# Kernel optimization log

Hardware: AMD Instinct MI355X
Metric: run time of the kernel (lower is better)

Reference implementation:

```python
import jax, jax.numpy as jnp
import numpy as np
from jax import lax

NEG = -1e30  # log-space 'zero' that stays finite for stable grads


def _logadd3(a, b, c):
    m = jnp.maximum(jnp.maximum(a, b), c)
    return m + jnp.log(jnp.exp(a - m) + jnp.exp(b - m) + jnp.exp(c - m))


def _logadd2(a, b):
    m = jnp.maximum(a, b)
    return m + jnp.log(jnp.exp(a - m) + jnp.exp(b - m))


def setup_inputs() -> dict:
    key = jax.random.key(0)
    k1, k2, k3 = jax.random.split(key, 3)
    B, T, V, L = 64, 2000, 512, 200
    logits = jax.random.normal(k1, (B, T, V), dtype=jnp.float32)
    # keep input lengths well above 2*L+1 so all paths are feasible
    input_lengths = (T - jax.random.randint(k2, (B,), 0, 256)).astype(jnp.int32)
    targets = jax.random.randint(k3, (B, L), 0, V, dtype=jnp.int32)  # 0 == pad == blank
    return {"logits": logits, "input_lengths": input_lengths, "targets": targets}


def ctc_loss_sum(logits, input_lengths, targets):
    B, T, V = logits.shape
    L = targets.shape[1]
    S = 2 * L + 1

    lp = jax.nn.log_softmax(logits, axis=-1)  # [B,T,V]

    # compact nonzero targets per row (masked_select equivalent, fixed shape)
    mask = targets != 0
    tlen = mask.sum(-1)  # [B] target_lengths
    pos = jnp.where(mask, jnp.cumsum(mask, axis=1) - 1, L)
    compact = jnp.zeros_like(targets).at[jnp.arange(B)[:, None], pos].set(targets, mode="drop")

    # extended label sequence: blank, y1, blank, y2, ..., blank  -> [B,S]
    s_idx = jnp.arange(S)
    lab_idx = jnp.clip((s_idx - 1) // 2, 0, L - 1)
    ext = jnp.where(s_idx % 2 == 1, compact[:, lab_idx], 0)  # [B,S]

    # skip transition s-2 -> s allowed iff label at s is non-blank and differs from s-2
    ext_m2 = jnp.pad(ext, ((0, 0), (2, 0)))[:, :S]
    skip_ok = (ext != 0) & (ext != ext_m2) & (s_idx >= 2)  # [B,S]

    lpT = jnp.transpose(lp, (1, 0, 2))  # [T,B,V], scan over time

    # init: alpha_0[0]=lp(blank), alpha_0[1]=lp(y1)
    lp0_ext = jnp.take_along_axis(lpT[0], ext[:, :2], axis=1)  # [B,2]
    alpha0 = jnp.full((B, S), NEG, dtype=lp.dtype).at[:, :2].set(lp0_ext)

    def step(alpha, inp):
        lp_t, t = inp
        a1 = jnp.pad(alpha, ((0, 0), (1, 0)), constant_values=NEG)[:, :S]
        a2 = jnp.pad(alpha, ((0, 0), (2, 0)), constant_values=NEG)[:, :S]
        a2 = jnp.where(skip_ok, a2, NEG)
        lp_e = jnp.take_along_axis(lp_t, ext, axis=1)  # [B,S]
        new = _logadd3(alpha, a1, a2) + lp_e
        active = (t < input_lengths)[:, None]
        return jnp.where(active, new, alpha), None

    alphaT, _ = lax.scan(step, alpha0, (lpT[1:], jnp.arange(1, T)))

    # read out at final blank (2*tlen) and final label (2*tlen-1)
    e1 = (2 * tlen)[:, None]
    e2 = (2 * tlen - 1)
    a1 = jnp.take_along_axis(alphaT, e1, axis=1)[:, 0]
    a2 = jnp.where(e2 >= 0,
                   jnp.take_along_axis(alphaT, jnp.clip(e2, 0)[:, None], axis=1)[:, 0],
                   NEG)
    ll = _logadd2(a1, a2)  # [B] log p(targets | logits)
    return -jnp.sum(ll)


def reference(logits, input_lengths, targets):
    return ctc_loss_sum(logits, input_lengths, targets)
```

## Files before the change

### kernel.cpp

```cpp
#include <hip/hip_runtime.h>

#define B_ 64
#define T_ 2000
#define V_ 512
#define L_ 200

typedef _Float16 half4 __attribute__((ext_vector_type(4)));

__device__ __forceinline__ float dpp_shr1_f(float x) {
  return __int_as_float(__builtin_amdgcn_update_dpp(0, __float_as_int(x), 0x138, 0xf, 0xf, true));
}
__device__ __forceinline__ int dpp_shr1_i(int x) {
  return __builtin_amdgcn_update_dpp(0, x, 0x138, 0xf, 0xf, true);
}
#define DPPADD(v, ctrl, rmask)                                                              \
  v += __int_as_float(__builtin_amdgcn_update_dpp(0, __float_as_int(v), ctrl, rmask, 0xf, true));


__global__ __launch_bounds__(64) void k0_compact(const int* __restrict__ targets,
                                                 int* __restrict__ compact,
                                                 int* __restrict__ tlen,
                                                 float* __restrict__ out) {
  const int b = blockIdx.x;
  const int lane = threadIdx.x;
  __shared__ int cbuf[256];
#pragma unroll
  for (int c = 0; c < 4; ++c) cbuf[c * 64 + lane] = 0;
  __syncthreads();
  int base = 0;
#pragma unroll
  for (int c = 0; c < 4; ++c) {
    const int l = c * 64 + lane;
    const int v = (l < L_) ? targets[b * L_ + l] : 0;
    const unsigned long long mk = __ballot(v != 0);
    const int pos = base + __popcll(mk & ((1ull << lane) - 1ull));
    if (v != 0) cbuf[pos] = v;
    base += __popcll(mk);
  }
  __syncthreads();
#pragma unroll
  for (int c = 0; c < 4; ++c) compact[b * 256 + c * 64 + lane] = cbuf[c * 64 + lane];
  if (lane == 0) {
    tlen[b] = base;
    if (b == 0) out[0] = 0.0f;
  }
}

__global__ __launch_bounds__(256) void k1_probs(float* __restrict__ logits,
                                                const int* __restrict__ compact,
                                                float* __restrict__ blank) {
  const int wave = threadIdx.x >> 6;
  const int lane = threadIdx.x & 63;
  const int r0 = (blockIdx.x * 4 + wave) * 2;
  const int b = r0 / T_;
  float* rp0 = logits + (size_t)r0 * V_;
  float* rp1 = rp0 + V_;
  const float4 xa0 = *(const float4*)(rp0 + 4 * lane);
  const float4 xa1 = *(const float4*)(rp0 + 256 + 4 * lane);
  const float4 xb0 = *(const float4*)(rp1 + 4 * lane);
  const float4 xb1 = *(const float4*)(rp1 + 256 + 4 * lane);
  const float ea0 = __expf(xa0.x), ea1 = __expf(xa0.y), ea2 = __expf(xa0.z), ea3 = __expf(xa0.w);
  const float ea4 = __expf(xa1.x), ea5 = __expf(xa1.y), ea6 = __expf(xa1.z), ea7 = __expf(xa1.w);
  const float eb0 = __expf(xb0.x), eb1 = __expf(xb0.y), eb2 = __expf(xb0.z), eb3 = __expf(xb0.w);
  const float eb4 = __expf(xb1.x), eb5 = __expf(xb1.y), eb6 = __expf(xb1.z), eb7 = __expf(xb1.w);
  float ra = ((ea0 + ea1) + (ea2 + ea3)) + ((ea4 + ea5) + (ea6 + ea7));
  float rb = ((eb0 + eb1) + (eb2 + eb3)) + ((eb4 + eb5) + (eb6 + eb7));
  DPPADD(ra, 0x111, 0xf); DPPADD(rb, 0x111, 0xf);
  DPPADD(ra, 0x112, 0xf); DPPADD(rb, 0x112, 0xf);
  DPPADD(ra, 0x114, 0xf); DPPADD(rb, 0x114, 0xf);
  DPPADD(ra, 0x118, 0xf); DPPADD(rb, 0x118, 0xf);
  DPPADD(ra, 0x142, 0xa); DPPADD(rb, 0x142, 0xa);
  DPPADD(ra, 0x143, 0xc); DPPADD(rb, 0x143, 0xc);
  const float suma = __int_as_float(__builtin_amdgcn_readlane(__float_as_int(ra), 63));
  const float sumb = __int_as_float(__builtin_amdgcn_readlane(__float_as_int(rb), 63));
  const float inva = 32.0f / suma;
  const float invb = 32.0f / sumb;
  __shared__ float prob[4][2][512];
  *(float4*)(&prob[wave][0][4 * lane]) = make_float4(ea0, ea1, ea2, ea3);
  *(float4*)(&prob[wave][0][256 + 4 * lane]) = make_float4(ea4, ea5, ea6, ea7);
  *(float4*)(&prob[wave][1][4 * lane]) = make_float4(eb0, eb1, eb2, eb3);
  *(float4*)(&prob[wave][1][256 + 4 * lane]) = make_float4(eb4, eb5, eb6, eb7);
  __syncthreads();
  const int4 c4 = *(const int4*)(compact + b * 256 + 4 * lane);
  const int l0 = 4 * lane;
  const bool v0 = l0 + 0 < L_, v1 = l0 + 1 < L_, v2 = l0 + 2 < L_, v3 = l0 + 3 < L_;
  half4 ha, hb;
  ha.x = (_Float16)(v0 ? prob[wave][0][c4.x] * inva : 0.0f);
  ha.y = (_Float16)(v1 ? prob[wave][0][c4.y] * inva : 0.0f);
  ha.z = (_Float16)(v2 ? prob[wave][0][c4.z] * inva : 0.0f);
  ha.w = (_Float16)(v3 ? prob[wave][0][c4.w] * inva : 0.0f);
  hb.x = (_Float16)(v0 ? prob[wave][1][c4.x] * invb : 0.0f);
  hb.y = (_Float16)(v1 ? prob[wave][1][c4.y] * invb : 0.0f);
  hb.z = (_Float16)(v2 ? prob[wave][1][c4.z] * invb : 0.0f);
  hb.w = (_Float16)(v3 ? prob[wave][1][c4.w] * invb : 0.0f);
  *(half4*)((char*)rp0 + 8 * lane) = ha;
  *(half4*)((char*)rp1 + 8 * lane) = hb;
  if (lane == 0) {
    const int t0 = r0 - b * T_;
    *(float2*)(blank + (b << 11) + t0) = make_float2(ea0 * inva, eb0 * invb);
  }
}

__global__ __launch_bounds__(64, 1) void k2_alpha(const float* __restrict__ pe,
                                                  const int* __restrict__ lens,
                                                  const int* __restrict__ compact,
                                                  const int* __restrict__ tlenp,
                                                  const float* __restrict__ blank,
                                                  float* __restrict__ out) {
  const int b = blockIdx.x;
  const int lane = threadIdx.x;
  const char* lbase = (const char*)(pe + (size_t)b * (T_ * V_)) + 8 * lane;
  const float* bl = blank + (b << 11);
  const int len = lens[b];

  const int4 c4 = *(const int4*)(compact + b * 256 + 4 * lane);
  const int cm1 = __shfl_up(c4.w, 1);
  const float m0 = (lane > 0 && c4.x != 0 && c4.x != cm1) ? 1.0f : 0.0f;
  const float m1 = (c4.y != 0 && c4.y != c4.x) ? 1.0f : 0.0f;
  const float m2 = (c4.z != 0 && c4.z != c4.y) ? 1.0f : 0.0f;
  const float m3 = (c4.w != 0 && c4.w != c4.z) ? 1.0f : 0.0f;

  float a0 = 0.f, a1 = 0.f, a2 = 0.f, a3 = 0.f, a4 = 0.f, a5 = 0.f, a6 = 0.f, a7 = 0.f;
  {
    const half4 h0 = *(const half4*)(lbase);
    const float pb0 = bl[0];
    if (lane == 0) { a0 = pb0; a1 = (float)h0.x; }
  }
  int E = 0;
  float fac = 1.0f;

  half4 LB0[8], LB1[8], LB2[8], LB3[8];
  float4 BLa0, BLa1, BLa2, BLa3, BLb0, BLb1, BLb2, BLb3;

#define LOADC(S, CIDX)                                                       \
  {                                                                          \
    int c8_ = (CIDX) * 8;                                                    \
    if (c8_ > T_ - 8) c8_ = T_ - 8;                                          \
    const char* rp_ = lbase + (size_t)c8_ * (V_ * 4);                        \
    _Pragma("unroll") for (int u = 0; u < 8; ++u)                            \
        LB##S[u] = *(const half4*)(rp_ + u * (V_ * 4));                      \
    BLa##S = *(const float4*)(bl + c8_);                                     \
    BLb##S = *(const float4*)(bl + c8_ + 4);                                 \
  }

#define STEP8(S, CIDX, ULO, MASKED)                                          \
  {                                                                          \
    const int tf_ = (CIDX) * 8;                                              \
    const float blv_[8] = {BLa##S.x, BLa##S.y, BLa##S.z, BLa##S.w,           \
                           BLb##S.x, BLb##S.y, BLb##S.z, BLb##S.w};          \
    _Pragma("unroll") for (int u = 0; u < 8; ++u) {                          \
      if (u >= (ULO)) {                                                      \
        const half4 hq = LB##S[u];                                           \
        const float qx = (float)hq.x, qy = (float)hq.y;                      \
        const float qz = (float)hq.z, qw = (float)hq.w;                      \
        const float pbv = blv_[u];                                           \
        const float s1 = dpp_shr1_f(a7) * fac;               \
        float n0 = (a0 + s1) * pbv;                                          \
        float n1 = fmaf(m0, s1, a0 + a1) * qx;                               \
        float n2 = (a2 + a1) * pbv;                                          \
        float n3 = fmaf(m1, a1, a2 + a3) * qy;                               \
        float n4 = (a4 + a3) * pbv;                                          \
        float n5 = fmaf(m2, a3, a4 + a5) * qz;                               \
        float n6 = (a6 + a5) * pbv;                                          \
        float n7 = fmaf(m3, a5, a6 + a7) * qw;                               \
        if (MASKED) {                                                        \
          const bool act = (tf_ + u) < len;                                  \
          n0 = act ? n0 : a0; n1 = act ? n1 : a1;                            \
          n2 = act ? n2 : a2; n3 = act ? n3 : a3;                            \
          n4 = act ? n4 : a4; n5 = act ? n5 : a5;                            \
          n6 = act ? n6 : a6; n7 = act ? n7 : a7;                            \
        }                                                                    \
        a0 = n0; a1 = n1; a2 = n2; a3 = n3;                                  \
        a4 = n4; a5 = n5; a6 = n6; a7 = n7;                                  \
      }                                                                      \
    }                                                                        \
  }

#define RENORM                                                               \
  {                                                                          \
    const float mx = fmaxf(fmaxf(fmaxf(a0, a1), fmaxf(a2, a3)),              \
                           fmaxf(fmaxf(a4, a5), fmaxf(a6, a7)));             \
    const bool dead = (mx == 0.0f);                                          \
    int e_ = (int)((__float_as_uint(mx) >> 23) & 0xff) - 127;                \
    if (dead) e_ = 0;                                                        \
    const float sc_ = __int_as_float((unsigned)(127 - e_) << 23);            \
    a0 *= sc_; a1 *= sc_; a2 *= sc_; a3 *= sc_;                              \
    a4 *= sc_; a5 *= sc_; a6 *= sc_; a7 *= sc_;                              \
    const int En_ = E + e_;                                                  \
    const int EnP_ = dpp_shr1_i(En_);                                        \
    E = dead ? EnP_ : En_;                                                   \
    const int Ep_ = dpp_shr1_i(E);                                           \
    const int d_ = Ep_ - E;                                                  \
    int dc_ = d_ < -126 ? -126 : (d_ > 126 ? 126 : d_);                      \
    fac = (d_ < -126) ? 0.0f : __int_as_float((unsigned)(dc_ + 127) << 23);  \
  }

  LOADC(0, 0); LOADC(1, 1); LOADC(2, 2); LOADC(3, 3);
  const int nfull = len >> 3;
  const int rem = len & 7;

  STEP8(0, 0, 1, 0);
  LOADC(0, 4);
  RENORM;

  int c = 1;
  while (c + 4 <= nfull) {
    STEP8(1, c, 0, 0);     LOADC(1, c + 4); RENORM;
    STEP8(2, c + 1, 0, 0); LOADC(2, c + 5); RENORM;
    STEP8(3, c + 2, 0, 0); LOADC(3, c + 6); RENORM;
    STEP8(0, c + 3, 0, 0); LOADC(0, c + 7); RENORM;
    c += 4;
  }
  while (c < nfull) {
    switch (c & 3) {
      case 0: STEP8(0, c, 0, 0); break;
      case 1: STEP8(1, c, 0, 0); break;
      case 2: STEP8(2, c, 0, 0); break;
      default: STEP8(3, c, 0, 0); break;
    }
    RENORM;
    c++;
  }
  if (rem) {
    switch (c & 3) {
      case 0: STEP8(0, c, 0, 1); break;
      case 1: STEP8(1, c, 0, 1); break;
      case 2: STEP8(2, c, 0, 1); break;
      default: STEP8(3, c, 0, 1); break;
    }
  }
#undef LOADC
#undef STEP8
#undef RENORM

  __shared__ float sval[512];
  __shared__ int sE[64];
  sval[lane * 8 + 0] = a0; sval[lane * 8 + 1] = a1;
  sval[lane * 8 + 2] = a2; sval[lane * 8 + 3] = a3;
  sval[lane * 8 + 4] = a4; sval[lane * 8 + 5] = a5;
  sval[lane * 8 + 6] = a6; sval[lane * 8 + 7] = a7;
  sE[lane] = E;
  __syncthreads();
  if (lane == 0) {
    const int tl = tlenp[b];
    const int e1 = 2 * tl;
    const int e2 = e1 - 1;
    const float v1 = sval[e1];
    const int E1 = sE[e1 >> 3];
    const float v2 = (e2 >= 0) ? sval[e2] : 0.0f;
    const int E2 = (e2 >= 0) ? sE[e2 >> 3] : E1;
    const int Em = (E1 > E2) ? E1 : E2;
    const float v = ldexpf(v1, E1 - Em) + ldexpf(v2, E2 - Em);
    const float ll = __logf(v) + (float)Em * 0.69314718056f - (float)len * 3.46573590280f;
    atomicAdd(out, -ll);
  }
}

extern "C" void kernel_launch(void* const* d_in, const int* in_sizes, int n_in,
                              void* d_out, int out_size, void* d_ws, size_t ws_size,
                              hipStream_t stream) {
  float* logits = (float*)d_in[0];
  const int* input_lengths = (const int*)d_in[1];
  const int* targets = (const int*)d_in[2];
  float* out = (float*)d_out;
  int* compact = (int*)d_ws;
  int* tlen = compact + B_ * 256;
  float* blank = (float*)((char*)d_ws + 131072);

  k0_compact<<<B_, 64, 0, stream>>>(targets, compact, tlen, out);
  k1_probs<<<(B_ * T_) / 8, 256, 0, stream>>>(logits, compact, blank);
  k2_alpha<<<B_, 64, 0, stream>>>(logits, input_lengths, compact, tlen, blank, out);
}
```

Before: 494.1 us.

## Store gathered label probs as fp32 and use a 16-step rolling prefetch ring

The gather kernel now writes the per-label probabilities as float4 (fp32) instead of packed fp16, so the alpha kernel reads full-precision values and skips the half-to-float conversions. The alpha recursion is restructured from four 8-row chunk buffers into a rolling ring of 16 per-timestep float4 registers. Each step reloads its slot with the row 16 steps ahead, and blank values are refilled in float4 groups. This doubles the bytes read from the intermediate buffer and changes how far ahead loads are issued, trading bandwidth and registers for a simpler, more evenly spaced prefetch schedule.

```diff
diff --git a/kernel.cpp b/kernel.cpp
--- a/kernel.cpp
+++ b/kernel.cpp
@@ -4,8 +4,6 @@
 #define T_ 2000
 #define V_ 512
 #define L_ 200
-
-typedef _Float16 half4 __attribute__((ext_vector_type(4)));
 
 __device__ __forceinline__ float dpp_shr1_f(float x) {
   return __int_as_float(__builtin_amdgcn_update_dpp(0, __float_as_int(x), 0x138, 0xf, 0xf, true));
@@ -84,17 +82,16 @@
   const int4 c4 = *(const int4*)(compact + b * 256 + 4 * lane);
   const int l0 = 4 * lane;
   const bool v0 = l0 + 0 < L_, v1 = l0 + 1 < L_, v2 = l0 + 2 < L_, v3 = l0 + 3 < L_;
-  half4 ha, hb;
-  ha.x = (_Float16)(v0 ? prob[wave][0][c4.x] * inva : 0.0f);
-  ha.y = (_Float16)(v1 ? prob[wave][0][c4.y] * inva : 0.0f);
-  ha.z = (_Float16)(v2 ? prob[wave][0][c4.z] * inva : 0.0f);
-  ha.w = (_Float16)(v3 ? prob[wave][0][c4.w] * inva : 0.0f);
-  hb.x = (_Float16)(v0 ? prob[wave][1][c4.x] * invb : 0.0f);
-  hb.y = (_Float16)(v1 ? prob[wave][1][c4.y] * invb : 0.0f);
-  hb.z = (_Float16)(v2 ? prob[wave][1][c4.z] * invb : 0.0f);
-  hb.w = (_Float16)(v3 ? prob[wave][1][c4.w] * invb : 0.0f);
-  *(half4*)((char*)rp0 + 8 * lane) = ha;
-  *(half4*)((char*)rp1 + 8 * lane) = hb;
+  const float4 ga = make_float4(v0 ? prob[wave][0][c4.x] * inva : 0.0f,
+                                v1 ? prob[wave][0][c4.y] * inva : 0.0f,
+                                v2 ? prob[wave][0][c4.z] * inva : 0.0f,
+                                v3 ? prob[wave][0][c4.w] * inva : 0.0f);
+  const float4 gb = make_float4(v0 ? prob[wave][1][c4.x] * invb : 0.0f,
+                                v1 ? prob[wave][1][c4.y] * invb : 0.0f,
+                                v2 ? prob[wave][1][c4.z] * invb : 0.0f,
+                                v3 ? prob[wave][1][c4.w] * invb : 0.0f);
+  *(float4*)(rp0 + 4 * lane) = ga;
+  *(float4*)(rp1 + 4 * lane) = gb;
   if (lane == 0) {
     const int t0 = r0 - b * T_;
     *(float2*)(blank + (b << 11) + t0) = make_float2(ea0 * inva, eb0 * invb);
@@ -109,11 +106,12 @@
                                                   float* __restrict__ out) {
   const int b = blockIdx.x;
   const int lane = threadIdx.x;
-  const char* lbase = (const char*)(pe + (size_t)b * (T_ * V_)) + 8 * lane;
+  const float* pb = pe + (size_t)b * (T_ * V_);
+  const int lo4 = 4 * lane;
   const float* bl = blank + (b << 11);
   const int len = lens[b];
 
-  const int4 c4 = *(const int4*)(compact + b * 256 + 4 * lane);
+  const int4 c4 = *(const int4*)(compact + b * 256 + lo4);
   const int cm1 = __shfl_up(c4.w, 1);
   const float m0 = (lane > 0 && c4.x != 0 && c4.x != cm1) ? 1.0f : 0.0f;
   const float m1 = (c4.y != 0 && c4.y != c4.x) ? 1.0f : 0.0f;
@@ -122,59 +120,20 @@
 
   float a0 = 0.f, a1 = 0.f, a2 = 0.f, a3 = 0.f, a4 = 0.f, a5 = 0.f, a6 = 0.f, a7 = 0.f;
   {
-    const half4 h0 = *(const half4*)(lbase);
+    const float4 h0 = *(const float4*)(pb + lo4);
     const float pb0 = bl[0];
-    if (lane == 0) { a0 = pb0; a1 = (float)h0.x; }
+    if (lane == 0) { a0 = pb0; a1 = h0.x; }
   }
   int E = 0;
   float fac = 1.0f;
 
-  half4 LB0[8], LB1[8], LB2[8], LB3[8];
-  float4 BLa0, BLa1, BLa2, BLa3, BLb0, BLb1, BLb2, BLb3;
-
-#define LOADC(S, CIDX)                                                       \
-  {                                                                          \
-    int c8_ = (CIDX) * 8;                                                    \
-    if (c8_ > T_ - 8) c8_ = T_ - 8;                                          \
-    const char* rp_ = lbase + (size_t)c8_ * (V_ * 4);                        \
-    _Pragma("unroll") for (int u = 0; u < 8; ++u)                            \
-        LB##S[u] = *(const half4*)(rp_ + u * (V_ * 4));                      \
-    BLa##S = *(const float4*)(bl + c8_);                                     \
-    BLb##S = *(const float4*)(bl + c8_ + 4);                                 \
-  }
-
-#define STEP8(S, CIDX, ULO, MASKED)                                          \
-  {                                                                          \
-    const int tf_ = (CIDX) * 8;                                              \
-    const float blv_[8] = {BLa##S.x, BLa##S.y, BLa##S.z, BLa##S.w,           \
-                           BLb##S.x, BLb##S.y, BLb##S.z, BLb##S.w};          \
-    _Pragma("unroll") for (int u = 0; u < 8; ++u) {                          \
-      if (u >= (ULO)) {                                                      \
-        const half4 hq = LB##S[u];                                           \
-        const float qx = (float)hq.x, qy = (float)hq.y;                      \
-        const float qz = (float)hq.z, qw = (float)hq.w;                      \
-        const float pbv = blv_[u];                                           \
-        const float s1 = dpp_shr1_f(a7) * fac;               \
-        float n0 = (a0 + s1) * pbv;                                          \
-        float n1 = fmaf(m0, s1, a0 + a1) * qx;                               \
-        float n2 = (a2 + a1) * pbv;                                          \
-        float n3 = fmaf(m1, a1, a2 + a3) * qy;                               \
-        float n4 = (a4 + a3) * pbv;                                          \
-        float n5 = fmaf(m2, a3, a4 + a5) * qz;                               \
-        float n6 = (a6 + a5) * pbv;                                          \
-        float n7 = fmaf(m3, a5, a6 + a7) * qw;                               \
-        if (MASKED) {                                                        \
-          const bool act = (tf_ + u) < len;                                  \
-          n0 = act ? n0 : a0; n1 = act ? n1 : a1;                            \
-          n2 = act ? n2 : a2; n3 = act ? n3 : a3;                            \
-          n4 = act ? n4 : a4; n5 = act ? n5 : a5;                            \
-          n6 = act ? n6 : a6; n7 = act ? n7 : a7;                            \
-        }                                                                    \
-        a0 = n0; a1 = n1; a2 = n2; a3 = n3;                                  \
-        a4 = n4; a5 = n5; a6 = n6; a7 = n7;                                  \
-      }                                                                      \
-    }                                                                        \
-  }
+  float4 LB[16];
+  float4 BL[4];
+
+#pragma unroll
+  for (int j = 0; j < 16; ++j) LB[j] = *(const float4*)(pb + (size_t)(1 + j) * V_ + lo4);
+#pragma unroll
+  for (int k = 0; k < 4; ++k) BL[k] = *(const float4*)(bl + 4 * k);
 
 #define RENORM                                                               \
   {                                                                          \
@@ -195,42 +154,50 @@
     fac = (d_ < -126) ? 0.0f : __int_as_float((unsigned)(dc_ + 127) << 23);  \
   }
 
-  LOADC(0, 0); LOADC(1, 1); LOADC(2, 2); LOADC(3, 3);
-  const int nfull = len >> 3;
-  const int rem = len & 7;
-
-  STEP8(0, 0, 1, 0);
-  LOADC(0, 4);
-  RENORM;
-
-  int c = 1;
-  while (c + 4 <= nfull) {
-    STEP8(1, c, 0, 0);     LOADC(1, c + 4); RENORM;
-    STEP8(2, c + 1, 0, 0); LOADC(2, c + 5); RENORM;
-    STEP8(3, c + 2, 0, 0); LOADC(3, c + 6); RENORM;
-    STEP8(0, c + 3, 0, 0); LOADC(0, c + 7); RENORM;
-    c += 4;
-  }
-  while (c < nfull) {
-    switch (c & 3) {
-      case 0: STEP8(0, c, 0, 0); break;
-      case 1: STEP8(1, c, 0, 0); break;
-      case 2: STEP8(2, c, 0, 0); break;
-      default: STEP8(3, c, 0, 0); break;
-    }
-    RENORM;
-    c++;
-  }
-  if (rem) {
-    switch (c & 3) {
-      case 0: STEP8(0, c, 0, 1); break;
-      case 1: STEP8(1, c, 0, 1); break;
-      case 2: STEP8(2, c, 0, 1); break;
-      default: STEP8(3, c, 0, 1); break;
-    }
-  }
-#undef LOADC
-#undef STEP8
+#define STEPJ(J, MASKED)                                                     \
+  {                                                                          \
+    const float4 q = LB[J];                                                  \
+    const float pbv = ((const float*)BL)[((((1 + J) >> 2) & 3) << 2) | ((1 + J) & 3)]; \
+    const float s1 = dpp_shr1_f(a7) * fac;                   \
+    float n0 = (a0 + s1) * pbv;                                              \
+    float n1 = fmaf(m0, s1, a0 + a1) * q.x;                                  \
+    float n2 = (a2 + a1) * pbv;                                              \
+    float n3 = fmaf(m1, a1, a2 + a3) * q.y;                                  \
+    float n4 = (a4 + a3) * pbv;                                              \
+    float n5 = fmaf(m2, a3, a4 + a5) * q.z;                                  \
+    float n6 = (a6 + a5) * pbv;                                              \
+    float n7 = fmaf(m3, a5, a6 + a7) * q.w;                                  \
+    if (MASKED) {                                                            \
+      const bool act = (t + J) < len;                                        \
+      n0 = act ? n0 : a0; n1 = act ? n1 : a1;                                \
+      n2 = act ? n2 : a2; n3 = act ? n3 : a3;                                \
+      n4 = act ? n4 : a4; n5 = act ? n5 : a5;                                \
+      n6 = act ? n6 : a6; n7 = act ? n7 : a7;                                \
+    }                                                                        \
+    a0 = n0; a1 = n1; a2 = n2; a3 = n3;                                      \
+    a4 = n4; a5 = n5; a6 = n6; a7 = n7;                                      \
+    if (((1 + J) & 3) == 3)                                                  \
+      BL[((1 + J) >> 2) & 3] =                                               \
+          *(const float4*)(bl + (t - 1) + 4 * (((1 + J) >> 2) + 4));         \
+    {                                                                        \
+      int rr = t + J + 16;                                                   \
+      rr = rr < T_ ? rr : T_ - 1;                                            \
+      LB[J] = *(const float4*)(pb + (size_t)rr * V_ + lo4);                  \
+    }                                                                        \
+    if ((J & 7) == 7) RENORM;                                                \
+  }
+
+  int t = 1;
+  while (t + 16 <= len) {
+#pragma unroll
+    for (int j = 0; j < 16; ++j) STEPJ(j, 0);
+    t += 16;
+  }
+  {
+#pragma unroll
+    for (int j = 0; j < 16; ++j) STEPJ(j, 1);
+  }
+#undef STEPJ
 #undef RENORM
 
   __shared__ float sval[512];
```

New measurement: 525.4 us. 1.06x slower.
